# Performance work log

Hardware: AMD Instinct MI355X
Metric: run time of the kernel (lower is better)

## Reference

```python
import jax, jax.numpy as jnp
import numpy as np

N0 = N1 = 50000
E = 800000
IN = 128
OUT = 128
H = 8
DK = OUT // H  # 16
SQRT_DK = float(np.sqrt(DK))
T = 2  # node types


def setup_inputs() -> dict:
    key = jax.random.key(0)
    ks = jax.random.split(key, 24)
    s = 1.0 / np.sqrt(IN)
    inp = {
        "feat0": jax.random.normal(ks[0], (N0, IN), jnp.float32),
        "feat1": jax.random.normal(ks[1], (N1, IN), jnp.float32),
        "ev0": jax.random.uniform(ks[2], (E,), jnp.float32),
        "ev1": jax.random.uniform(ks[3], (E,), jnp.float32),
        "ev2": jax.random.uniform(ks[4], (E,), jnp.float32),
        "src0": jax.random.randint(ks[5], (E,), 0, N0),   # t0 -> t1
        "dst0": jax.random.randint(ks[6], (E,), 0, N1),
        "src1": jax.random.randint(ks[7], (E,), 0, N1),   # t1 -> t0
        "dst1": jax.random.randint(ks[8], (E,), 0, N0),
        "src2": jax.random.randint(ks[9], (E,), 0, N0),   # t0 -> t0
        "dst2": jax.random.randint(ks[10], (E,), 0, N0),
        # per-node-type parameters, stacked over T types
        "Kw": jax.random.normal(ks[11], (T, IN, OUT), jnp.float32) * s,
        "Kb": jnp.zeros((T, OUT), jnp.float32),
        "Qw": jax.random.normal(ks[12], (T, IN, OUT), jnp.float32) * s,
        "Qb": jnp.zeros((T, OUT), jnp.float32),
        "Vw": jax.random.normal(ks[13], (T, IN, OUT), jnp.float32) * s,
        "Vb": jnp.zeros((T, OUT), jnp.float32),
        "Aw": jax.random.normal(ks[14], (T, OUT, OUT), jnp.float32) * s,
        "Ab": jnp.zeros((T, OUT), jnp.float32),
        "ew": jax.random.normal(ks[15], (), jnp.float32),  # e_linear weight (1x1)
        "eb": jnp.zeros((), jnp.float32),                  # e_linear bias
        "skip": jnp.ones((T,), jnp.float32),
    }
    return inp


def _etype_agg(feat_s, feat_d, ts, td, src, dst, ev, n_dst,
               Kw, Kb, Qw, Qb, Vw, Vb, ew, eb):
    """One canonical etype: gather q.k per edge, edge_softmax over dst, u_mul_e + sum."""
    k = (feat_s @ Kw[ts] + Kb[ts]).reshape(-1, H, DK)
    v = (feat_s @ Vw[ts] + Vb[ts]).reshape(-1, H, DK)
    q = (feat_d @ Qw[td] + Qb[td]).reshape(-1, H, DK)
    # per-edge dot(q[dst], k[src]) over d_k -> [E, H]
    score = jnp.einsum('ehd,ehd->eh', q[dst], k[src])
    ea = ev[:, None] * ew + eb                     # e_linear on scalar edge feature, [E,1]
    score = score * ea / SQRT_DK                   # [E, H]
    # segmented softmax over incoming edges per destination node, per head
    m = jax.ops.segment_max(score, dst, num_segments=n_dst)
    ex = jnp.exp(score - m[dst])
    z = jax.ops.segment_sum(ex, dst, num_segments=n_dst)
    attn = ex / z[dst]                             # [E, H]
    msg = v[src] * attn[:, :, None]                # [E, H, DK]
    return jax.ops.segment_sum(msg, dst, num_segments=n_dst)  # [n_dst, H, DK]


def reference(feat0, feat1, ev0, ev1, ev2, src0, dst0, src1, dst1, src2, dst2,
              Kw, Kb, Qw, Qb, Vw, Vb, Aw, Ab, ew, eb, skip):
    # etype (t0,e0,t1)
    agg1 = _etype_agg(feat0, feat1, 0, 1, src0, dst0, ev0, N1,
                      Kw, Kb, Qw, Qb, Vw, Vb, ew, eb)
    # etypes targeting t0: (t1,e1,t0) and (t0,e2,t0); cross_reducer='mean'
    agg0a = _etype_agg(feat1, feat0, 1, 0, src1, dst1, ev1, N0,
                       Kw, Kb, Qw, Qb, Vw, Vb, ew, eb)
    agg0b = _etype_agg(feat0, feat0, 0, 0, src2, dst2, ev2, N0,
                       Kw, Kb, Qw, Qb, Vw, Vb, ew, eb)
    agg0 = 0.5 * (agg0a + agg0b)

    def _out(agg, feat, nid):
        t = agg.reshape(-1, OUT)
        trans = t @ Aw[nid] + Ab[nid]              # dropout omitted (eval mode)
        alpha = jax.nn.sigmoid(skip[nid])
        return trans * alpha + feat * (1.0 - alpha)

    h0 = _out(agg0, feat0, 0)
    h1 = _out(agg1, feat1, 1)
    return (h0, h1)
```

## Files before the change

kernel.cpp:

```cpp
#include <hip/hip_runtime.h>
#include <hip/hip_bf16.h>
#include <hip/hip_fp16.h>
#include <math.h>


#define NDIM 128
#define NRNG 32
#define NBK 512
#define UNITS (NBK * 4)
#define HSPAN 2048

typedef __attribute__((ext_vector_type(8))) short short8;
typedef __attribute__((ext_vector_type(4))) float f32x4;

__device__ __forceinline__ float bf2f(unsigned short u) {
    union { unsigned int i; float f; } x; x.i = ((unsigned int)u) << 16; return x.f;
}
__device__ __forceinline__ unsigned short f2bf(float f) {
    unsigned int u = __float_as_uint(f);
    unsigned int r = (u + 0x7FFFu + ((u >> 16) & 1u)) >> 16;
    return (unsigned short)r;
}
__device__ __forceinline__ int range_of(int d, int n) {
    return (int)(((long long)d * NRNG) / n);
}

__global__ void wt_prep(const float* __restrict__ Kw, const float* __restrict__ Qw,
                        const float* __restrict__ Vw, const float* __restrict__ Aw,
                        unsigned short* __restrict__ Wtbuf)
{
    const int b = blockIdx.x;
    const int t = b >> 2, m = b & 3;
    const float* src = (m == 0 ? Kw : m == 1 ? Qw : m == 2 ? Vw : Aw) + (size_t)t * 16384;
    unsigned short* dst = Wtbuf + (size_t)b * 16384;
    for (int i = threadIdx.x; i < 16384; i += blockDim.x) {
        const int k = i >> 7, nn = i & 127;
        dst[nn * 128 + k] = f2bf(src[i]);
    }
}

__global__ __launch_bounds__(256) void gemm_kqv(
    const float* __restrict__ feat0, const float* __restrict__ feat1,
    const unsigned short* __restrict__ Wtbuf,
    const float* __restrict__ Kb, const float* __restrict__ Qb, const float* __restrict__ Vb,
    unsigned short* __restrict__ K0o, unsigned short* __restrict__ Q0o, unsigned short* __restrict__ V0o,
    unsigned short* __restrict__ K1o, unsigned short* __restrict__ Q1o, unsigned short* __restrict__ V1o,
    int n0, int n1, int blocks0)
{
    const int b = blockIdx.x;
    const bool t1 = (b >= blocks0);
    const float* feat = t1 ? feat1 : feat0;
    const int n = t1 ? n1 : n0;
    const int boff = t1 ? NDIM : 0;
    const unsigned short* Wt = Wtbuf + (t1 ? 4 * 16384 : 0);
    unsigned short* outs[3];
    outs[0] = t1 ? K1o : K0o; outs[1] = t1 ? Q1o : Q0o; outs[2] = t1 ? V1o : V0o;
    const float* biases[3] = {Kb + boff, Qb + boff, Vb + boff};

    const int tid = threadIdx.x;
    const int w = tid >> 6, lane = tid & 63;
    const int r16 = lane & 15, kg = lane >> 4;
    const int wrow = (t1 ? b - blocks0 : b) * 64 + w * 16;
    const int arow = min(wrow + r16, n - 1);

    short8 afr[4];
#pragma unroll
    for (int k0i = 0; k0i < 4; ++k0i) {
        const float* ap = feat + (size_t)arow * NDIM + k0i * 32 + kg * 8;
        const float4 lo = *(const float4*)ap;
        const float4 hi = *(const float4*)(ap + 4);
        short8 a;
        a[0] = (short)f2bf(lo.x); a[1] = (short)f2bf(lo.y);
        a[2] = (short)f2bf(lo.z); a[3] = (short)f2bf(lo.w);
        a[4] = (short)f2bf(hi.x); a[5] = (short)f2bf(hi.y);
        a[6] = (short)f2bf(hi.z); a[7] = (short)f2bf(hi.w);
        afr[k0i] = a;
    }
#pragma unroll
    for (int m = 0; m < 3; ++m) {
        const unsigned short* wt = Wt + (size_t)m * 16384;
        f32x4 acc[8];
#pragma unroll
        for (int c = 0; c < 8; ++c) acc[c] = (f32x4){0.f, 0.f, 0.f, 0.f};
#pragma unroll
        for (int k0i = 0; k0i < 4; ++k0i)
#pragma unroll
            for (int c = 0; c < 8; ++c) {
                const short8 bb = *(const short8*)(wt + (size_t)(16 * c + r16) * NDIM + k0i * 32 + kg * 8);
                acc[c] = __builtin_amdgcn_mfma_f32_16x16x32_bf16(afr[k0i], bb, acc[c], 0, 0, 0);
            }
#pragma unroll
        for (int c = 0; c < 8; ++c) {
            const int col = 16 * c + r16;
            const float bb = biases[m][col];
#pragma unroll
            for (int j = 0; j < 4; ++j) {
                const int row = wrow + kg * 4 + j;
                if (row < n) outs[m][(size_t)row * NDIM + col] = f2bf(acc[c][j] + bb);
            }
        }
    }
}

__global__ __launch_bounds__(256) void gemm_out(
    const unsigned short* __restrict__ aggb0a, const unsigned short* __restrict__ aggb0b,
    const unsigned short* __restrict__ aggb1,
    const unsigned short* __restrict__ Wtbuf, const float* __restrict__ Ab,
    const float* __restrict__ feat0, const float* __restrict__ feat1,
    const float* __restrict__ skip, float* __restrict__ out,
    int n0, int n1, int blocks0)
{
    const int b = blockIdx.x;
    const bool t1 = (b >= blocks0);
    const int n = t1 ? n1 : n0;
    const unsigned short* A1 = t1 ? aggb1 : aggb0a;
    const unsigned short* A2 = t1 ? (const unsigned short*)nullptr : aggb0b;
    const unsigned short* Wt = Wtbuf + (t1 ? 7 : 3) * 16384;
    const float* bias = Ab + (t1 ? NDIM : 0);
    const float* feat = t1 ? feat1 : feat0;
    float* C = out + (t1 ? (size_t)n0 * NDIM : 0);
    const int nid = t1 ? 1 : 0;

    const int tid = threadIdx.x;
    const int w = tid >> 6, lane = tid & 63;
    const int r16 = lane & 15, kg = lane >> 4;
    const int wrow = (t1 ? b - blocks0 : b) * 64 + w * 16;
    const int arow = min(wrow + r16, n - 1);

    short8 afr[4];
#pragma unroll
    for (int k0i = 0; k0i < 4; ++k0i) {
        short8 a = *(const short8*)(A1 + (size_t)arow * NDIM + k0i * 32 + kg * 8);
        if (!t1) {
            const short8 bb = *(const short8*)(A2 + (size_t)arow * NDIM + k0i * 32 + kg * 8);
#pragma unroll
            for (int j = 0; j < 8; ++j) {
                const float v = 0.5f * (bf2f((unsigned short)a[j]) + bf2f((unsigned short)bb[j]));
                a[j] = (short)f2bf(v);
            }
        }
        afr[k0i] = a;
    }
    f32x4 acc[8];
#pragma unroll
    for (int c = 0; c < 8; ++c) acc[c] = (f32x4){0.f, 0.f, 0.f, 0.f};
#pragma unroll
    for (int k0i = 0; k0i < 4; ++k0i)
#pragma unroll
        for (int c = 0; c < 8; ++c) {
            const short8 bb = *(const short8*)(Wt + (size_t)(16 * c + r16) * NDIM + k0i * 32 + kg * 8);
            acc[c] = __builtin_amdgcn_mfma_f32_16x16x32_bf16(afr[k0i], bb, acc[c], 0, 0, 0);
        }
    const float sk = skip[nid];
    const float alpha = 1.f / (1.f + __expf(-sk));
    const float beta = 1.f - alpha;
#pragma unroll
    for (int c = 0; c < 8; ++c) {
        const int col = 16 * c + r16;
        const float bb = bias[col];
#pragma unroll
        for (int j = 0; j < 4; ++j) {
            const int row = wrow + kg * 4 + j;
            if (row < n)
                C[(size_t)row * NDIM + col] = (acc[c][j] + bb) * alpha + feat[(size_t)row * NDIM + col] * beta;
        }
    }
}

__global__ __launch_bounds__(256) void bucket_count(
    const int* __restrict__ d0, int E0, const int* __restrict__ d1, int E1,
    const int* __restrict__ d2, int E2, int n0, int n1, int* __restrict__ cnts)
{
    const int seg = blockIdx.y;
    const int* dst = seg == 0 ? d0 : (seg == 1 ? d1 : d2);
    const int E = seg == 0 ? E0 : (seg == 1 ? E1 : E2);
    const int ns = seg == 0 ? n1 : n0;
    const int unit = blockIdx.x * 4 + (threadIdx.x >> 6);
    const int lane = threadIdx.x & 63;
    const int span = (E + UNITS - 1) / UNITS;
    const int b = unit * span;
    const int e = min(b + span, E);

    int run[NRNG];
#pragma unroll
    for (int r0 = 0; r0 < NRNG; ++r0) run[r0] = 0;
    for (int i0 = b; i0 < e; i0 += 64) {
        const int i = i0 + lane;
        const bool v = i < e;
        const int d = v ? dst[i] : 0;
        const unsigned int r = v ? (unsigned int)range_of(d, ns) : 0xFFu;
#pragma unroll
        for (int r0 = 0; r0 < NRNG; ++r0)
            run[r0] += __popcll(__ballot(r == (unsigned int)r0));
    }
    if (lane == 0) {
        int* c = cnts + ((size_t)seg * UNITS + unit) * NRNG;
#pragma unroll
        for (int r0 = 0; r0 < NRNG; ++r0) c[r0] = run[r0];
    }
}

__global__ __launch_bounds__(256) void bucket_scan(int* __restrict__ cnts, int* __restrict__ rcur)
{
    const int seg = blockIdx.x >> 5;
    const int r = blockIdx.x & 31;
    const int t = threadIdx.x, lane = t & 63, w = t >> 6;

    int v[8];
    int run = 0;
#pragma unroll
    for (int j = 0; j < 8; ++j) {
        const int u = t * 8 + j;
        const int x = cnts[((size_t)seg * UNITS + u) * NRNG + r];
        v[j] = run;
        run += x;
    }
    const int tsum = run;
    int x = tsum;
#pragma unroll
    for (int o = 1; o < 64; o <<= 1) {
        const int y = __shfl_up(x, o);
        if (lane >= o) x += y;
    }
    const int wexc = x - tsum;
    __shared__ int wsum[4];
    if (lane == 63) wsum[w] = x;
    __syncthreads();
    int wbase = 0;
    for (int i = 0; i < w; ++i) wbase += wsum[i];
    const int base = wbase + wexc;
#pragma unroll
    for (int j = 0; j < 8; ++j) {
        const int u = t * 8 + j;
        cnts[((size_t)seg * UNITS + u) * NRNG + r] = base + v[j];
    }
    if (t == 255) rcur[seg * NRNG + r] = base + tsum;
}

__global__ __launch_bounds__(256) void bucket_write(
    const int* __restrict__ d0, const int* __restrict__ s0, const float* __restrict__ e0, int E0,
    const int* __restrict__ d1, const int* __restrict__ s1, const float* __restrict__ e1, int E1,
    const int* __restrict__ d2, const int* __restrict__ s2, const float* __restrict__ e2, int E2,
    int n0, int n1, const float* __restrict__ ew, const float* __restrict__ eb,
    const int* __restrict__ cnts, uint2* __restrict__ stg, int cap)
{
    const int seg = blockIdx.y;
    const int* dst = seg == 0 ? d0 : (seg == 1 ? d1 : d2);
    const int* src = seg == 0 ? s0 : (seg == 1 ? s1 : s2);
    const float* ev = seg == 0 ? e0 : (seg == 1 ? e1 : e2);
    const int E = seg == 0 ? E0 : (seg == 1 ? E1 : E2);
    const int ns = seg == 0 ? n1 : n0;
    const int unit = blockIdx.x * 4 + (threadIdx.x >> 6);
    const int lane = threadIdx.x & 63;
    const int span = (E + UNITS - 1) / UNITS;
    const int b = unit * span;
    const int e = min(b + span, E);
    const float LOG2E = 1.4426950408889634f;
    const float ews = ew[0] * 0.25f * LOG2E;
    const float ebs = eb[0] * 0.25f * LOG2E;
    uint2* sbase = stg + (size_t)seg * NRNG * cap;

    int run[NRNG];
    {
        const int* c = cnts + ((size_t)seg * UNITS + unit) * NRNG;
#pragma unroll
        for (int r0 = 0; r0 < NRNG; ++r0) run[r0] = c[r0];
    }
    for (int i0 = b; i0 < e; i0 += 64) {
        const int i = i0 + lane;
        const bool v = i < e;
        int d = 0, s = 0; float ee = 0.f;
        if (v) { d = dst[i]; s = src[i]; ee = ev[i]; }
        const unsigned int r = v ? (unsigned int)range_of(d, ns) : 0xFFu;
#pragma unroll
        for (int r0 = 0; r0 < NRNG; ++r0) {
            const unsigned long long m = __ballot(r == (unsigned int)r0);
            if (m == 0ull) continue;
            if (r == (unsigned int)r0) {
                const int off = run[r0] + __popcll(m & ((1ull << lane) - 1ull));
                sbase[(size_t)r0 * cap + off] =
                    make_uint2((unsigned int)d | ((unsigned int)s << 16), __float_as_uint(ee * ews + ebs));
            }
            run[r0] += __popcll(m);
        }
    }
}

__global__ __launch_bounds__(1024) void sortB(
    const uint2* __restrict__ stg, int cap, const int* __restrict__ rcur,
    int nA, int* __restrict__ offA, unsigned int* __restrict__ gA,
    int nB, int* __restrict__ offB, unsigned int* __restrict__ gB,
    int nC, int* __restrict__ offC, unsigned int* __restrict__ gC)
{
    const int seg = blockIdx.y;
    const int r = blockIdx.x;
    const int n = seg == 0 ? nA : (seg == 1 ? nB : nC);
    int* off = seg == 0 ? offA : (seg == 1 ? offB : offC);
    unsigned int* edg = seg == 0 ? gA : (seg == 1 ? gB : gC);
    const int cnt = rcur[seg * NRNG + r];
    const uint2* s = stg + ((size_t)seg * NRNG + r) * cap;
    const int dbase = (int)(((long long)r * n + NRNG - 1) / NRNG);
    const int dnext = (int)(((long long)(r + 1) * n + NRNG - 1) / NRNG);
    const int span = dnext - dbase;
    int ebase = 0;
    for (int i = 0; i < r; ++i) ebase += rcur[seg * NRNG + i];

    __shared__ int hist[HSPAN];
    __shared__ int wsum[16];
    const int tid = threadIdx.x, lane = tid & 63, wid = tid >> 6;

    for (int i = tid; i < span; i += 1024) hist[i] = 0;
    __syncthreads();
    for (int i = tid; i < cnt; i += 1024)
        atomicAdd(&hist[(int)(s[i].x & 0xFFFFu) - dbase], 1);
    __syncthreads();
    const int C = (span + 1023) >> 10;
    int v[4];
    int run = 0;
    const int b0 = tid * C;
#pragma unroll 4
    for (int j = 0; j < C; ++j) {
        const int i = b0 + j;
        const int x = (i < span) ? hist[i] : 0;
        v[j] = run;
        run += x;
    }
    int x = run;
#pragma unroll
    for (int o = 1; o < 64; o <<= 1) {
        const int y = __shfl_up(x, o);
        if (lane >= o) x += y;
    }
    if (lane == 63) wsum[wid] = x;
    __syncthreads();
    int wbase = 0;
    for (int i = 0; i < wid; ++i) wbase += wsum[i];
    const int tb = ebase + wbase + (x - run);
#pragma unroll 4
    for (int j = 0; j < C; ++j) {
        const int i = b0 + j;
        if (i < span) hist[i] = tb + v[j];
    }
    __syncthreads();
    for (int i = tid; i < span; i += 1024) off[dbase + i] = hist[i];
    if (r == NRNG - 1 && tid == 0) off[n] = ebase + cnt;
    __syncthreads();
    for (int i = tid; i < cnt; i += 1024) {
        const uint2 e = s[i];
        const int d = (int)(e.x & 0xFFFFu);
        const int p = atomicAdd(&hist[d - dbase], 1);
        const float wf = __uint_as_float(e.y);
        const __half hh = __float2half(wf);
        edg[p] = (e.x >> 16) | ((unsigned int)__half_as_ushort(hh) << 16);
    }
}

__global__ __launch_bounds__(256) void edge_agg3(
    const int* __restrict__ off0, const unsigned int* __restrict__ edg0,
    const unsigned short* __restrict__ K0e, const unsigned short* __restrict__ Q0e,
    const unsigned short* __restrict__ V0e, unsigned short* __restrict__ out0, int nd0,
    const int* __restrict__ off1, const unsigned int* __restrict__ edg1,
    const unsigned short* __restrict__ K1e, const unsigned short* __restrict__ Q1e,
    const unsigned short* __restrict__ V1e, unsigned short* __restrict__ out1, int nd1,
    const int* __restrict__ off2, const unsigned int* __restrict__ edg2,
    const unsigned short* __restrict__ K2e, const unsigned short* __restrict__ Q2e,
    const unsigned short* __restrict__ V2e, unsigned short* __restrict__ out2, int nd2)
{
    const int seg = blockIdx.y;
    const int* off = seg == 0 ? off0 : (seg == 1 ? off1 : off2);
    const unsigned int* edg = seg == 0 ? edg0 : (seg == 1 ? edg1 : edg2);
    const unsigned short* K = seg == 0 ? K0e : (seg == 1 ? K1e : K2e);
    const unsigned short* Q = seg == 0 ? Q0e : (seg == 1 ? Q1e : Q2e);
    const unsigned short* V = seg == 0 ? V0e : (seg == 1 ? V1e : V2e);
    unsigned short* aggb = seg == 0 ? out0 : (seg == 1 ? out1 : out2);
    const int n_dst = seg == 0 ? nd0 : (seg == 1 ? nd1 : nd2);

    const int wv = (blockIdx.x * blockDim.x + threadIdx.x) >> 6;
    const int lane = threadIdx.x & 63;
    const int half = lane >> 5, l5 = lane & 31;
    const int dst = 2 * wv + half;
    const bool valid = dst < n_dst;
    int beg = 0, len = 0;
    if (valid) { beg = off[dst]; len = off[dst + 1] - beg; }
    const int maxLen = max(len, __shfl_xor(len, 32));
    if (maxLen == 0) {
        if (valid) *(ushort4*)(aggb + (size_t)dst * NDIM + 4 * l5) = (ushort4){0, 0, 0, 0};
        return;
    }
    float qx = 0.f, qy = 0.f, qz = 0.f, qw = 0.f;
    if (valid) {
        const ushort4 qr = *(const ushort4*)(Q + (size_t)dst * NDIM + 4 * l5);
        qx = bf2f(qr.x); qy = bf2f(qr.y); qz = bf2f(qr.z); qw = bf2f(qr.w);
    }
    float z = 0.f, a0 = 0.f, a1 = 0.f, a2 = 0.f, a3 = 0.f;

    unsigned int ec = (l5 < len) ? edg[beg + l5] : 0u;
    for (int t0 = 0; t0 < maxLen; t0 += 32) {
        unsigned int en = 0u;
        const int t0n = t0 + 32;
        if (t0n < maxLen && t0n + l5 < len) en = edg[beg + t0n + l5];
        const int lim = min(32, maxLen - t0);
        for (int u = 0; u < lim; ++u) {
            const int sl = (half << 5) + u;
            const unsigned int vv = (unsigned int)__shfl((int)ec, sl);
            const int s = (int)(vv & 0xFFFFu);
            const float w = __half2float(__ushort_as_half((unsigned short)(vv >> 16)));
            const bool act = (t0 + u) < len;
            const ushort4 kr = *(const ushort4*)(K + (size_t)s * NDIM + 4 * l5);
            const ushort4 vr = *(const ushort4*)(V + (size_t)s * NDIM + 4 * l5);
            float d = qx * bf2f(kr.x) + qy * bf2f(kr.y) + qz * bf2f(kr.z) + qw * bf2f(kr.w);
            d += __shfl_xor(d, 1);
            d += __shfl_xor(d, 2);
            const float p = act ? exp2f(d * w) : 0.f;
            z += p;
            a0 += p * bf2f(vr.x);
            a1 += p * bf2f(vr.y);
            a2 += p * bf2f(vr.z);
            a3 += p * bf2f(vr.w);
        }
        ec = en;
    }
    if (valid) {
        const float inv = (len > 0) ? 1.f / z : 0.f;
        ushort4 o;
        o.x = f2bf(a0 * inv); o.y = f2bf(a1 * inv);
        o.z = f2bf(a2 * inv); o.w = f2bf(a3 * inv);
        *(ushort4*)(aggb + (size_t)dst * NDIM + 4 * l5) = o;
    }
}

extern "C" void kernel_launch(void* const* d_in, const int* in_sizes, int n_in,
                              void* d_out, int out_size, void* d_ws, size_t ws_size,
                              hipStream_t stream)
{
    const float* feat0 = (const float*)d_in[0];
    const float* feat1 = (const float*)d_in[1];
    const float* ev0 = (const float*)d_in[2];
    const float* ev1 = (const float*)d_in[3];
    const float* ev2 = (const float*)d_in[4];
    const int* src0 = (const int*)d_in[5];
    const int* dst0 = (const int*)d_in[6];
    const int* src1 = (const int*)d_in[7];
    const int* dst1 = (const int*)d_in[8];
    const int* src2 = (const int*)d_in[9];
    const int* dst2 = (const int*)d_in[10];
    const float* Kw = (const float*)d_in[11];
    const float* Kb = (const float*)d_in[12];
    const float* Qw = (const float*)d_in[13];
    const float* Qb = (const float*)d_in[14];
    const float* Vw = (const float*)d_in[15];
    const float* Vb = (const float*)d_in[16];
    const float* Aw = (const float*)d_in[17];
    const float* Ab = (const float*)d_in[18];
    const float* ew = (const float*)d_in[19];
    const float* eb = (const float*)d_in[20];
    const float* skip = (const float*)d_in[21];

    const int n0 = in_sizes[0] / NDIM;
    const int n1 = in_sizes[1] / NDIM;
    const int E0 = in_sizes[5];
    const int E1 = in_sizes[7];
    const int E2 = in_sizes[9];
    if (max(n0, n1) > 65504) return;
    const int Emax = max(E0, max(E1, E2));
    const int cap = Emax / NRNG + 8192;

    auto rup = [](size_t b) { return (b + 255) & ~size_t(255); };
    const size_t need =
        rup((size_t)8 * 16384 * 2) +
        rup((size_t)n0 * NDIM * 2) * 3 +
        rup((size_t)n1 * NDIM * 2) * 3 +
        rup((size_t)n1 * NDIM * 2) +
        rup((size_t)n0 * NDIM * 2) * 2 +
        rup((size_t)(n1 + 1) * 4) +
        rup((size_t)(n0 + 1) * 4) * 2 +
        rup((size_t)128 * 4) +
        rup((size_t)3 * UNITS * NRNG * 4) +
        rup((size_t)3 * NRNG * cap * 8) +
        rup((size_t)E0 * 4) + rup((size_t)E1 * 4) + rup((size_t)E2 * 4);
    if (ws_size < need) return;

    char* p = (char*)d_ws;
    auto alloc = [&](size_t bytes) -> char* {
        char* r = p;
        p += (bytes + 255) & ~size_t(255);
        return r;
    };
    unsigned short* Wtbuf = (unsigned short*)alloc((size_t)8 * 16384 * 2);
    unsigned short* K0 = (unsigned short*)alloc((size_t)n0 * NDIM * 2);
    unsigned short* Q0 = (unsigned short*)alloc((size_t)n0 * NDIM * 2);
    unsigned short* V0 = (unsigned short*)alloc((size_t)n0 * NDIM * 2);
    unsigned short* K1 = (unsigned short*)alloc((size_t)n1 * NDIM * 2);
    unsigned short* Q1 = (unsigned short*)alloc((size_t)n1 * NDIM * 2);
    unsigned short* V1 = (unsigned short*)alloc((size_t)n1 * NDIM * 2);
    unsigned short* aggb1  = (unsigned short*)alloc((size_t)n1 * NDIM * 2);
    unsigned short* aggb0a = (unsigned short*)alloc((size_t)n0 * NDIM * 2);
    unsigned short* aggb0b = (unsigned short*)alloc((size_t)n0 * NDIM * 2);
    int* off0 = (int*)alloc((size_t)(n1 + 1) * 4);
    int* off1 = (int*)alloc((size_t)(n0 + 1) * 4);
    int* off2 = (int*)alloc((size_t)(n0 + 1) * 4);
    int* rcur = (int*)alloc((size_t)128 * 4);
    int* cnts = (int*)alloc((size_t)3 * UNITS * NRNG * 4);
    uint2* stg = (uint2*)alloc((size_t)3 * NRNG * cap * 8);
    unsigned int* edg0 = (unsigned int*)alloc((size_t)E0 * 4);
    unsigned int* edg1 = (unsigned int*)alloc((size_t)E1 * 4);
    unsigned int* edg2 = (unsigned int*)alloc((size_t)E2 * 4);

    dim3 blk(256);
    const int blocks0 = (n0 + 63) / 64, blocks1 = (n1 + 63) / 64;

    wt_prep<<<8, 256, 0, stream>>>(Kw, Qw, Vw, Aw, Wtbuf);
    gemm_kqv<<<blocks0 + blocks1, blk, 0, stream>>>(feat0, feat1, Wtbuf, Kb, Qb, Vb,
                                                    K0, Q0, V0, K1, Q1, V1, n0, n1, blocks0);

    bucket_count<<<dim3(NBK, 3), blk, 0, stream>>>(dst0, E0, dst1, E1, dst2, E2, n0, n1, cnts);
    bucket_scan<<<3 * NRNG, blk, 0, stream>>>(cnts, rcur);
    bucket_write<<<dim3(NBK, 3), blk, 0, stream>>>(dst0, src0, ev0, E0,
                                                   dst1, src1, ev1, E1,
                                                   dst2, src2, ev2, E2,
                                                   n0, n1, ew, eb, cnts, stg, cap);
    sortB<<<dim3(NRNG, 3), 1024, 0, stream>>>(stg, cap, rcur,
                                              n1, off0, edg0,
                                              n0, off1, edg1,
                                              n0, off2, edg2);

    const int nmax = (n0 > n1) ? n0 : n1;
    const int ebx = ((nmax + 1) / 2 + 3) / 4;
    edge_agg3<<<dim3(ebx, 3), blk, 0, stream>>>(
        off0, edg0, K0, Q1, V0, aggb1, n1,
        off1, edg1, K1, Q0, V1, aggb0a, n0,
        off2, edg2, K0, Q0, V0, aggb0b, n0);

    gemm_out<<<blocks0 + blocks1, blk, 0, stream>>>(aggb0a, aggb0b, aggb1, Wtbuf, Ab,
                                                    feat0, feat1, skip, (float*)d_out,
                                                    n0, n1, blocks0);
}
```

Baseline: 451.1 us.

## Stage GEMM epilogues through shared memory and unroll edge aggregation by two

Both GEMM kernels (QKV projection and output transform) now write MFMA accumulators to a padded shared-memory tile and reread them so that each lane emits contiguous 8-element vector stores, replacing scattered 2-byte and 4-byte column stores. The residual feat read in the output kernel also becomes vectorized. The edge-aggregation loop processes two edges per iteration with separate accumulators, aiming for more memory-level parallelism on the K/V gathers. This costs extra LDS (about 33KB per block), added barriers, and higher register pressure in the aggregation kernel.

```diff
diff --git a/kernel.cpp b/kernel.cpp
--- a/kernel.cpp
+++ b/kernel.cpp
@@ -60,8 +60,10 @@
     const int tid = threadIdx.x;
     const int w = tid >> 6, lane = tid & 63;
     const int r16 = lane & 15, kg = lane >> 4;
-    const int wrow = (t1 ? b - blocks0 : b) * 64 + w * 16;
-    const int arow = min(wrow + r16, n - 1);
+    const int brow = (t1 ? b - blocks0 : b) * 64;
+    const int arow = min(brow + w * 16 + r16, n - 1);
+
+    __shared__ float sacc[64][129];
 
     short8 afr[4];
 #pragma unroll
@@ -76,6 +78,7 @@
         a[6] = (short)f2bf(hi.z); a[7] = (short)f2bf(hi.w);
         afr[k0i] = a;
     }
+    const int c8 = (lane & 15) * 8;
 #pragma unroll
     for (int m = 0; m < 3; ++m) {
         const unsigned short* wt = Wt + (size_t)m * 16384;
@@ -89,14 +92,26 @@
                 const short8 bb = *(const short8*)(wt + (size_t)(16 * c + r16) * NDIM + k0i * 32 + kg * 8);
                 acc[c] = __builtin_amdgcn_mfma_f32_16x16x32_bf16(afr[k0i], bb, acc[c], 0, 0, 0);
             }
-#pragma unroll
-        for (int c = 0; c < 8; ++c) {
-            const int col = 16 * c + r16;
-            const float bb = biases[m][col];
-#pragma unroll
-            for (int j = 0; j < 4; ++j) {
-                const int row = wrow + kg * 4 + j;
-                if (row < n) outs[m][(size_t)row * NDIM + col] = f2bf(acc[c][j] + bb);
+        __syncthreads();
+#pragma unroll
+        for (int c = 0; c < 8; ++c)
+#pragma unroll
+            for (int j = 0; j < 4; ++j)
+                sacc[w * 16 + kg * 4 + j][16 * c + r16] = acc[c][j];
+        __syncthreads();
+        const float4 blo = *(const float4*)(biases[m] + c8);
+        const float4 bhi = *(const float4*)(biases[m] + c8 + 4);
+        const float bias8[8] = {blo.x, blo.y, blo.z, blo.w, bhi.x, bhi.y, bhi.z, bhi.w};
+#pragma unroll
+        for (int j = 0; j < 4; ++j) {
+            const int rloc = w * 16 + (lane >> 4) + j * 4;
+            const int grow = brow + rloc;
+            if (grow < n) {
+                short8 o;
+#pragma unroll
+                for (int i = 0; i < 8; ++i)
+                    o[i] = (short)f2bf(sacc[rloc][c8 + i] + bias8[i]);
+                *(short8*)(outs[m] + (size_t)grow * NDIM + c8) = o;
             }
         }
     }
@@ -124,8 +139,10 @@
     const int tid = threadIdx.x;
     const int w = tid >> 6, lane = tid & 63;
     const int r16 = lane & 15, kg = lane >> 4;
-    const int wrow = (t1 ? b - blocks0 : b) * 64 + w * 16;
-    const int arow = min(wrow + r16, n - 1);
+    const int brow = (t1 ? b - blocks0 : b) * 64;
+    const int arow = min(brow + w * 16 + r16, n - 1);
+
+    __shared__ float sacc[64][129];
 
     short8 afr[4];
 #pragma unroll
@@ -151,18 +168,38 @@
             const short8 bb = *(const short8*)(Wt + (size_t)(16 * c + r16) * NDIM + k0i * 32 + kg * 8);
             acc[c] = __builtin_amdgcn_mfma_f32_16x16x32_bf16(afr[k0i], bb, acc[c], 0, 0, 0);
         }
+    __syncthreads();
+#pragma unroll
+    for (int c = 0; c < 8; ++c)
+#pragma unroll
+        for (int j = 0; j < 4; ++j)
+            sacc[w * 16 + kg * 4 + j][16 * c + r16] = acc[c][j];
+    __syncthreads();
+
     const float sk = skip[nid];
     const float alpha = 1.f / (1.f + __expf(-sk));
     const float beta = 1.f - alpha;
-#pragma unroll
-    for (int c = 0; c < 8; ++c) {
-        const int col = 16 * c + r16;
-        const float bb = bias[col];
-#pragma unroll
-        for (int j = 0; j < 4; ++j) {
-            const int row = wrow + kg * 4 + j;
-            if (row < n)
-                C[(size_t)row * NDIM + col] = (acc[c][j] + bb) * alpha + feat[(size_t)row * NDIM + col] * beta;
+    const int c8 = (lane & 15) * 8;
+    const float4 blo = *(const float4*)(bias + c8);
+    const float4 bhi = *(const float4*)(bias + c8 + 4);
+#pragma unroll
+    for (int j = 0; j < 4; ++j) {
+        const int rloc = w * 16 + (lane >> 4) + j * 4;
+        const int grow = brow + rloc;
+        if (grow < n) {
+            const float4 fa = *(const float4*)(feat + (size_t)grow * NDIM + c8);
+            const float4 fb = *(const float4*)(feat + (size_t)grow * NDIM + c8 + 4);
+            float4 oa, ob;
+            oa.x = (sacc[rloc][c8 + 0] + blo.x) * alpha + fa.x * beta;
+            oa.y = (sacc[rloc][c8 + 1] + blo.y) * alpha + fa.y * beta;
+            oa.z = (sacc[rloc][c8 + 2] + blo.z) * alpha + fa.z * beta;
+            oa.w = (sacc[rloc][c8 + 3] + blo.w) * alpha + fa.w * beta;
+            ob.x = (sacc[rloc][c8 + 4] + bhi.x) * alpha + fb.x * beta;
+            ob.y = (sacc[rloc][c8 + 5] + bhi.y) * alpha + fb.y * beta;
+            ob.z = (sacc[rloc][c8 + 6] + bhi.z) * alpha + fb.z * beta;
+            ob.w = (sacc[rloc][c8 + 7] + bhi.w) * alpha + fb.w * beta;
+            *(float4*)(C + (size_t)grow * NDIM + c8) = oa;
+            *(float4*)(C + (size_t)grow * NDIM + c8 + 4) = ob;
         }
     }
 }
@@ -392,7 +429,8 @@
         const ushort4 qr = *(const ushort4*)(Q + (size_t)dst * NDIM + 4 * l5);
         qx = bf2f(qr.x); qy = bf2f(qr.y); qz = bf2f(qr.z); qw = bf2f(qr.w);
     }
-    float z = 0.f, a0 = 0.f, a1 = 0.f, a2 = 0.f, a3 = 0.f;
+    float zA = 0.f, aA0 = 0.f, aA1 = 0.f, aA2 = 0.f, aA3 = 0.f;
+    float zB = 0.f, aB0 = 0.f, aB1 = 0.f, aB2 = 0.f, aB3 = 0.f;
 
     unsigned int ec = (l5 < len) ? edg[beg + l5] : 0u;
     for (int t0 = 0; t0 < maxLen; t0 += 32) {
@@ -400,31 +438,43 @@
         const int t0n = t0 + 32;
         if (t0n < maxLen && t0n + l5 < len) en = edg[beg + t0n + l5];
         const int lim = min(32, maxLen - t0);
-        for (int u = 0; u < lim; ++u) {
-            const int sl = (half << 5) + u;
-            const unsigned int vv = (unsigned int)__shfl((int)ec, sl);
-            const int s = (int)(vv & 0xFFFFu);
-            const float w = __half2float(__ushort_as_half((unsigned short)(vv >> 16)));
-            const bool act = (t0 + u) < len;
-            const ushort4 kr = *(const ushort4*)(K + (size_t)s * NDIM + 4 * l5);
-            const ushort4 vr = *(const ushort4*)(V + (size_t)s * NDIM + 4 * l5);
-            float d = qx * bf2f(kr.x) + qy * bf2f(kr.y) + qz * bf2f(kr.z) + qw * bf2f(kr.w);
-            d += __shfl_xor(d, 1);
-            d += __shfl_xor(d, 2);
-            const float p = act ? exp2f(d * w) : 0.f;
-            z += p;
-            a0 += p * bf2f(vr.x);
-            a1 += p * bf2f(vr.y);
-            a2 += p * bf2f(vr.z);
-            a3 += p * bf2f(vr.w);
+        for (int u = 0; u < lim; u += 2) {
+            const int sl0 = (half << 5) + u;
+            const unsigned int v0 = (unsigned int)__shfl((int)ec, sl0);
+            const unsigned int v1 = (unsigned int)__shfl((int)ec, sl0 + 1);
+            const bool act0 = (t0 + u) < len;
+            const bool act1 = (u + 1 < lim) && ((t0 + u + 1) < len);
+            const int s0 = (int)(v0 & 0xFFFFu);
+            const int s1 = (int)(v1 & 0xFFFFu);
+            const float w0 = __half2float(__ushort_as_half((unsigned short)(v0 >> 16)));
+            const float w1 = __half2float(__ushort_as_half((unsigned short)(v1 >> 16)));
+            const ushort4 kr0 = *(const ushort4*)(K + (size_t)s0 * NDIM + 4 * l5);
+            const ushort4 vr0 = *(const ushort4*)(V + (size_t)s0 * NDIM + 4 * l5);
+            const ushort4 kr1 = *(const ushort4*)(K + (size_t)s1 * NDIM + 4 * l5);
+            const ushort4 vr1 = *(const ushort4*)(V + (size_t)s1 * NDIM + 4 * l5);
+            float d0 = qx * bf2f(kr0.x) + qy * bf2f(kr0.y) + qz * bf2f(kr0.z) + qw * bf2f(kr0.w);
+            float d1 = qx * bf2f(kr1.x) + qy * bf2f(kr1.y) + qz * bf2f(kr1.z) + qw * bf2f(kr1.w);
+            d0 += __shfl_xor(d0, 1);
+            d1 += __shfl_xor(d1, 1);
+            d0 += __shfl_xor(d0, 2);
+            d1 += __shfl_xor(d1, 2);
+            const float p0 = act0 ? exp2f(d0 * w0) : 0.f;
+            const float p1 = act1 ? exp2f(d1 * w1) : 0.f;
+            zA += p0;
+            aA0 += p0 * bf2f(vr0.x); aA1 += p0 * bf2f(vr0.y);
+            aA2 += p0 * bf2f(vr0.z); aA3 += p0 * bf2f(vr0.w);
+            zB += p1;
+            aB0 += p1 * bf2f(vr1.x); aB1 += p1 * bf2f(vr1.y);
+            aB2 += p1 * bf2f(vr1.z); aB3 += p1 * bf2f(vr1.w);
         }
         ec = en;
     }
     if (valid) {
+        const float z = zA + zB;
         const float inv = (len > 0) ? 1.f / z : 0.f;
         ushort4 o;
-        o.x = f2bf(a0 * inv); o.y = f2bf(a1 * inv);
-        o.z = f2bf(a2 * inv); o.w = f2bf(a3 * inv);
+        o.x = f2bf((aA0 + aB0) * inv); o.y = f2bf((aA1 + aB1) * inv);
+        o.z = f2bf((aA2 + aB2) * inv); o.w = f2bf((aA3 + aB3) * inv);
         *(ushort4*)(aggb + (size_t)dst * NDIM + 4 * l5) = o;
     }
 }
```

Measured after the change: 419.3 us. 7.1% less time.
